# Optimization experiments

Hardware: AMD Instinct MI355X
Metric: run time of the kernel (lower is better)

The kernel has to match this reference:

```python
import jax, jax.numpy as jnp
import numpy as np

B, S, H = 4, 2048, 1024
HEADS = 16
DFF = 4 * H
EPS = 1e-12


def _layer_norm(x, w, b):
    mu = jnp.mean(x, axis=-1, keepdims=True)
    var = jnp.mean(jnp.square(x - mu), axis=-1, keepdims=True)
    return (x - mu) * jax.lax.rsqrt(var + EPS) * w + b


def setup_inputs() -> dict:
    key = jax.random.key(0)
    ks = jax.random.split(key, 12)
    sc = 0.02
    return {
        "input": jax.random.normal(ks[0], (B, S, H), dtype=jnp.float32),
        "input_mask": jnp.zeros((B, 1, 1, S), dtype=jnp.float32),
        "norm_w": jnp.ones((H,), jnp.float32),
        "norm_b": jnp.zeros((H,), jnp.float32),
        "qkv_w": sc * jax.random.normal(ks[1], (H, 3 * H), jnp.float32),
        "qkv_b": jnp.zeros((3 * H,), jnp.float32),
        "attn_ow": sc * jax.random.normal(ks[2], (H, H), jnp.float32),
        "attn_ob": jnp.zeros((H,), jnp.float32),
        "attn_nw": jnp.ones((H,), jnp.float32),
        "attn_nb": jnp.zeros((H,), jnp.float32),
        "inter_w": sc * jax.random.normal(ks[3], (H, DFF), jnp.float32),
        "inter_b": jnp.zeros((DFF,), jnp.float32),
        "output_w": sc * jax.random.normal(ks[4], (DFF, H), jnp.float32),
        "output_b": jnp.zeros((H,), jnp.float32),
    }


def reference(input, input_mask, norm_w, norm_b, qkv_w, qkv_b, attn_ow, attn_ob,
              attn_nw, attn_nb, inter_w, inter_b, output_w, output_b):
    b, s, h = input.shape
    hd = h // HEADS
    # pre-LN + fused QKV projection (qkv_func)
    x_ln = _layer_norm(input, norm_w, norm_b)
    qkv = x_ln @ qkv_w + qkv_b                      # [b, s, 3h]
    qkv = qkv.reshape(b, s, 3, HEADS, hd)
    q, k, v = qkv[:, :, 0], qkv[:, :, 1], qkv[:, :, 2]   # [b, s, heads, hd]
    # scaled dot-product attention (flash_attn equivalent, non-causal)
    scale = 1.0 / jnp.sqrt(jnp.float32(hd))
    scores = jnp.einsum('bqnd,bknd->bnqk', q, k) * scale  # [b, heads, s, s]
    scores = scores + input_mask                           # additive mask
    probs = jax.nn.softmax(scores, axis=-1)
    ctx = jnp.einsum('bnqk,bknd->bqnd', probs, v).reshape(b, s, h)
    # attention output projection + residual (mlp_func first half)
    attn_out = ctx @ attn_ow + attn_ob + input
    # post-attention LN + FFN (GELU) + residual
    y = _layer_norm(attn_out, attn_nw, attn_nb)
    y = jax.nn.gelu(y @ inter_w + inter_b, approximate=False)
    return y @ output_w + output_b + attn_out
```

## Files before the change

### kernel.cpp

```cpp
#include <hip/hip_runtime.h>
#include <math.h>

typedef __bf16 bf16_t;
typedef bf16_t bf16x8 __attribute__((ext_vector_type(8)));
typedef bf16_t bf16x4 __attribute__((ext_vector_type(4)));
typedef float f32x4 __attribute__((ext_vector_type(4)));
typedef float f32x16 __attribute__((ext_vector_type(16)));

#define BB 4
#define SS 2048
#define HD1 1024
#define NH 16
#define DFF_ 4096

__device__ __forceinline__ void gload_lds16(const bf16_t* g, bf16_t* l) {
  __builtin_amdgcn_global_load_lds(
      (const __attribute__((address_space(1))) void*)g,
      (__attribute__((address_space(3))) void*)l, 16, 0, 0);
}

__device__ __forceinline__ unsigned pack2_bf16(float a, float b) {
  union { bf16_t h[2]; unsigned u; } cv;
  cv.h[0] = (bf16_t)a;
  cv.h[1] = (bf16_t)b;
  return cv.u;
}

__device__ __forceinline__ float block_reduce_sum(float v, float* red) {
  const int lane = threadIdx.x & 63;
  const int wid = threadIdx.x >> 6;
#pragma unroll
  for (int off = 32; off > 0; off >>= 1) v += __shfl_down(v, off, 64);
  if (lane == 0) red[wid] = v;
  __syncthreads();
  float s = red[0] + red[1] + red[2] + red[3];
  __syncthreads();
  return s;
}

__global__ __launch_bounds__(256) void ln_kernel(const float* __restrict__ x,
                                                 const float* __restrict__ w,
                                                 const float* __restrict__ bv,
                                                 bf16_t* __restrict__ out) {
  __shared__ float red[4];
  const size_t row = blockIdx.x;
  const float4 xv = *(const float4*)(x + row * HD1 + threadIdx.x * 4);
  float s = xv.x + xv.y + xv.z + xv.w;
  s = block_reduce_sum(s, red);
  const float mu = s * (1.0f / HD1);
  float4 d;
  d.x = xv.x - mu; d.y = xv.y - mu; d.z = xv.z - mu; d.w = xv.w - mu;
  float sq = d.x * d.x + d.y * d.y + d.z * d.z + d.w * d.w;
  sq = block_reduce_sum(sq, red);
  const float rs = rsqrtf(sq * (1.0f / HD1) + 1e-12f);
  const float4 wv = *(const float4*)(w + threadIdx.x * 4);
  const float4 bb = *(const float4*)(bv + threadIdx.x * 4);
  bf16x4 o;
  o[0] = (bf16_t)(d.x * rs * wv.x + bb.x);
  o[1] = (bf16_t)(d.y * rs * wv.y + bb.y);
  o[2] = (bf16_t)(d.z * rs * wv.z + bb.z);
  o[3] = (bf16_t)(d.w * rs * wv.w + bb.w);
  *(bf16x4*)(out + row * HD1 + threadIdx.x * 4) = o;
}

__global__ __launch_bounds__(256) void wt_kernel(const float* __restrict__ W,
                                                 bf16_t* __restrict__ Wt,
                                                 int K, int N) {
  __shared__ bf16_t T[32][33];
  const int t = threadIdx.x;
  const int n0 = blockIdx.x * 32, k0 = blockIdx.y * 32;
  const int a = t >> 5, c = t & 31;
#pragma unroll
  for (int i = 0; i < 4; ++i) {
    const int kl = a + i * 8;
    T[kl][c] = (bf16_t)W[(size_t)(k0 + kl) * N + n0 + c];
  }
  __syncthreads();
#pragma unroll
  for (int i = 0; i < 4; ++i) {
    const int nl = a + i * 8;
    Wt[(size_t)(n0 + nl) * K + k0 + c] = T[c][nl];
  }
}

__global__ __launch_bounds__(256) void vtrans_kernel(const bf16_t* __restrict__ qkv,
                                                     bf16_t* __restrict__ Vt) {
  const int t = threadIdx.x;
  const int s = blockIdx.x * 256 + t;
  const int head = blockIdx.y, b = blockIdx.z;
  const bf16_t* src = qkv + (size_t)(b * SS + s) * 3072 + 2048 + head * 64;
  bf16_t* dst = Vt + ((size_t)(b * NH + head) * 64) * SS + s;
#pragma unroll
  for (int j = 0; j < 8; ++j) {
    bf16x8 v = *(const bf16x8*)(src + j * 8);
#pragma unroll
    for (int e = 0; e < 8; ++e) dst[(size_t)(j * 8 + e) * SS] = v[e];
  }
}

template <int EPI, bool OBF>
__global__ __launch_bounds__(256) void gemm_bf16(
    const bf16_t* __restrict__ A, const bf16_t* __restrict__ Wt,
    const float* __restrict__ bias, const float* __restrict__ R,
    void* __restrict__ Cout, int M, int N, int K) {
  __shared__ __align__(16) char smem[65536];
  bf16_t* As = (bf16_t*)smem;
  bf16_t* Bs = (bf16_t*)(smem + 32768);
  const int tid = threadIdx.x;
  const int lane = tid & 63;
  const int w = tid >> 6;
  const int wm = (w >> 1) * 64, wn = (w & 1) * 64;
  const int l15 = lane & 15, l4 = lane >> 4;

  const int gx = gridDim.x;
  int id = blockIdx.x + gx * blockIdx.y;
  const int cpx = (gx * gridDim.y) >> 3;
  id = (id & 7) * cpx + (id >> 3);
  const int m0 = (id / gx) * 128;
  const int n0 = (id % gx) * 128;

  const int lrow = tid >> 3;
  const int lcol = (tid & 7) * 8;
  const bf16_t* Ag = A + (size_t)(m0 + lrow) * K + lcol;
  const bf16_t* Bg = Wt + (size_t)(n0 + lrow) * K + lcol;
  const size_t rstride = (size_t)32 * K;

#pragma unroll
  for (int c = 0; c < 4; ++c) {
    gload_lds16(Ag + c * rstride, As + c * 2048 + w * 512);
    gload_lds16(Bg + c * rstride, Bs + c * 2048 + w * 512);
  }

  const int NT = K >> 6;
  f32x4 acc[4][4] = {};

  for (int t = 0; t < NT; ++t) {
    const int cur = t & 1;
    __syncthreads();
    if (t + 1 < NT) {
      const bf16_t* Agn = Ag + (size_t)(t + 1) * 64;
      const bf16_t* Bgn = Bg + (size_t)(t + 1) * 64;
      bf16_t* Ad = As + (cur ^ 1) * 8192;
      bf16_t* Bd = Bs + (cur ^ 1) * 8192;
#pragma unroll
      for (int c = 0; c < 4; ++c) {
        gload_lds16(Agn + c * rstride, Ad + c * 2048 + w * 512);
        gload_lds16(Bgn + c * rstride, Bd + c * 2048 + w * 512);
      }
    }
    const bf16_t* Ab = As + cur * 8192;
    const bf16_t* Bb = Bs + cur * 8192;
    bf16x8 af[2][4], bfr[2][4];
#pragma unroll
    for (int ks = 0; ks < 2; ++ks) {
#pragma unroll
      for (int i = 0; i < 4; ++i)
        af[ks][i] =
            *(const bf16x8*)(Ab + (wm + i * 16 + l15) * 64 + ks * 32 + l4 * 8);
#pragma unroll
      for (int j = 0; j < 4; ++j)
        bfr[ks][j] =
            *(const bf16x8*)(Bb + (wn + j * 16 + l15) * 64 + ks * 32 + l4 * 8);
    }
#pragma unroll
    for (int ks = 0; ks < 2; ++ks)
#pragma unroll
      for (int i = 0; i < 4; ++i)
#pragma unroll
        for (int j = 0; j < 4; ++j)
          acc[i][j] = __builtin_amdgcn_mfma_f32_16x16x32_bf16(
              af[ks][i], bfr[ks][j], acc[i][j], 0, 0, 0);
  }

  if (OBF) {
    __syncthreads();
    float* Cs = (float*)smem;
#pragma unroll
    for (int j = 0; j < 4; ++j) {
      const float bj = bias[n0 + wn + j * 16 + l15];
#pragma unroll
      for (int i = 0; i < 4; ++i)
#pragma unroll
        for (int r = 0; r < 4; ++r) {
          float v = acc[i][j][r] + bj;
          if (EPI == 1)
            v = 0.5f * v * (1.0f + erff(v * 0.70710678118654752440f));
          Cs[(wm + i * 16 + l4 * 4 + r) * 128 + wn + j * 16 + l15] = v;
        }
    }
    __syncthreads();
    bf16_t* Cb = (bf16_t*)Cout;
#pragma unroll
    for (int p = 0; p < 16; ++p) {
      const int idx = p * 256 + tid;
      const int row = idx >> 5, c4 = idx & 31;
      const f32x4 v = *(const f32x4*)(Cs + row * 128 + c4 * 4);
      bf16x4 o;
      o[0] = (bf16_t)v[0]; o[1] = (bf16_t)v[1];
      o[2] = (bf16_t)v[2]; o[3] = (bf16_t)v[3];
      *(bf16x4*)(Cb + (size_t)(m0 + row) * N + n0 + c4 * 4) = o;
    }
  } else {
    float* Cf = (float*)Cout;
#pragma unroll
    for (int j = 0; j < 4; ++j) {
      const int gn = n0 + wn + j * 16 + l15;
      const float bj = bias[gn];
#pragma unroll
      for (int i = 0; i < 4; ++i) {
        const int gm = m0 + wm + i * 16 + l4 * 4;
#pragma unroll
        for (int r = 0; r < 4; ++r) {
          float v = acc[i][j][r] + bj;
          if (EPI == 2) v += R[(size_t)(gm + r) * N + gn];
          Cf[(size_t)(gm + r) * N + gn] = v;
        }
      }
    }
  }
}

__global__ __launch_bounds__(256, 2) void attn_kernel(
    const bf16_t* __restrict__ qkv, const bf16_t* __restrict__ Vt,
    const float* __restrict__ mask, bf16_t* __restrict__ ctx) {
  __shared__ __align__(16) bf16_t K_lds[64 * 72];
  __shared__ __align__(16) bf16_t Vt_lds[64 * 72];
  const int tid = threadIdx.x;
  const int lane = tid & 63;
  const int w = tid >> 6;
  const int l31 = lane & 31;
  const int h = lane >> 5;
  const int q0 = blockIdx.x * 128;
  const int head = blockIdx.y;
  const int b = blockIdx.z;
  const int qrow = q0 + w * 32 + l31;

  bf16x8 qf[4];
  {
    const bf16_t* qp = qkv + (size_t)(b * SS + qrow) * 3072 + head * 64 + 8 * h;
#pragma unroll
    for (int ks = 0; ks < 4; ++ks) qf[ks] = *(const bf16x8*)(qp + 16 * ks);
  }

  const int srow = tid >> 2;
  const int scol = (tid & 3) * 16;

  float m = -3.0e38f, l = 0.0f;
  f32x16 cacc0 = {};
  f32x16 cacc1 = {};

  for (int kv0 = 0; kv0 < SS; kv0 += 64) {
    const bf16_t* kp =
        qkv + (size_t)(b * SS + kv0 + srow) * 3072 + 1024 + head * 64 + scol;
    const bf16_t* vp =
        Vt + ((size_t)(b * NH + head) * 64 + srow) * SS + kv0 + scol;
    const bf16x8 k0 = *(const bf16x8*)kp;
    const bf16x8 k1 = *(const bf16x8*)(kp + 8);
    const bf16x8 v0 = *(const bf16x8*)vp;
    const bf16x8 v1 = *(const bf16x8*)(vp + 8);
    float4 mv[8];
#pragma unroll
    for (int k2 = 0; k2 < 8; ++k2)
      mv[k2] = *(const float4*)(mask + (size_t)b * SS + kv0 + 8 * k2 + 4 * h);
    __syncthreads();
    *(bf16x8*)(K_lds + srow * 72 + scol) = k0;
    *(bf16x8*)(K_lds + srow * 72 + scol + 8) = k1;
    *(bf16x8*)(Vt_lds + srow * 72 + scol) = v0;
    *(bf16x8*)(Vt_lds + srow * 72 + scol + 8) = v1;
    __syncthreads();

    f32x16 sacc0 = {};
    f32x16 sacc1 = {};
#pragma unroll
    for (int ks = 0; ks < 4; ++ks) {
      const bf16x8 kf0 = *(const bf16x8*)(K_lds + l31 * 72 + 16 * ks + 8 * h);
      const bf16x8 kf1 =
          *(const bf16x8*)(K_lds + (l31 + 32) * 72 + 16 * ks + 8 * h);
      sacc0 = __builtin_amdgcn_mfma_f32_32x32x16_bf16(kf0, qf[ks], sacc0, 0, 0, 0);
      sacc1 = __builtin_amdgcn_mfma_f32_32x32x16_bf16(kf1, qf[ks], sacc1, 0, 0, 0);
    }

    float ps[32];
    float tmax = -3.0e38f;
#pragma unroll
    for (int r = 0; r < 16; ++r) {
      const float s0 = sacc0[r] * 0.125f + mv[(r >> 2)][r & 3];
      const float s1 = sacc1[r] * 0.125f + mv[(r >> 2) + 4][r & 3];
      ps[r] = s0;
      ps[16 + r] = s1;
      tmax = fmaxf(tmax, fmaxf(s0, s1));
    }
    tmax = fmaxf(tmax, __shfl_xor(tmax, 32, 64));
    if (__any(tmax > m + 8.0f)) {
      const float mnew = fmaxf(m, tmax);
      const float sc = __expf(m - mnew);
      m = mnew;
      l *= sc;
#pragma unroll
      for (int r = 0; r < 16; ++r) {
        const float scr = __shfl(sc, (r & 3) + 8 * (r >> 2) + 4 * h, 64);
        cacc0[r] *= scr;
        cacc1[r] *= scr;
      }
    }
    float ls = 0.0f;
#pragma unroll
    for (int i = 0; i < 32; ++i) {
      ps[i] = __expf(ps[i] - m);
      ls += ps[i];
    }
    l += ls + __shfl_xor(ls, 32, 64);

    unsigned pw0[8], pw1[8];
#pragma unroll
    for (int k = 0; k < 8; ++k) {
      const int base = (k >> 2) * 16 + (k & 3) * 4;
      pw0[k] = pack2_bf16(ps[base + 0], ps[base + 1]);
      pw1[k] = pack2_bf16(ps[base + 2], ps[base + 3]);
    }
#pragma unroll
    for (int t = 0; t < 4; ++t) {
      const unsigned e0 = h ? pw0[2 * t] : pw0[2 * t + 1];
      const unsigned e1 = h ? pw1[2 * t] : pw1[2 * t + 1];
      const unsigned o0 = (unsigned)__shfl_xor((int)e0, 32, 64);
      const unsigned o1 = (unsigned)__shfl_xor((int)e1, 32, 64);
      const unsigned a0 = h ? pw0[2 * t + 1] : pw0[2 * t];
      const unsigned a1 = h ? pw1[2 * t + 1] : pw1[2 * t];
      union { unsigned u[4]; bf16x8 v; } pu;
      pu.u[0] = h ? o0 : a0;
      pu.u[1] = h ? o1 : a1;
      pu.u[2] = h ? a0 : o0;
      pu.u[3] = h ? a1 : o1;
      const bf16x8 vf0 = *(const bf16x8*)(Vt_lds + l31 * 72 + 16 * t + 8 * h);
      const bf16x8 vf1 =
          *(const bf16x8*)(Vt_lds + (l31 + 32) * 72 + 16 * t + 8 * h);
      cacc0 = __builtin_amdgcn_mfma_f32_32x32x16_bf16(pu.v, vf0, cacc0, 0, 0, 0);
      cacc1 = __builtin_amdgcn_mfma_f32_32x32x16_bf16(pu.v, vf1, cacc1, 0, 0, 0);
    }
  }

  const float linv = 1.0f / l;
#pragma unroll
  for (int r = 0; r < 16; ++r) {
    const int rq = (r & 3) + 8 * (r >> 2) + 4 * h;
    const float li = __shfl(linv, rq, 64);
    const int grow = q0 + w * 32 + rq;
    bf16_t* op = ctx + (size_t)(b * SS + grow) * 1024 + head * 64 + l31;
    op[0] = (bf16_t)(cacc0[r] * li);
    op[32] = (bf16_t)(cacc1[r] * li);
  }
}

extern "C" void kernel_launch(void* const* d_in, const int* in_sizes, int n_in,
                              void* d_out, int out_size, void* d_ws, size_t ws_size,
                              hipStream_t stream) {
  const float* input    = (const float*)d_in[0];
  const float* mask     = (const float*)d_in[1];
  const float* norm_w   = (const float*)d_in[2];
  const float* norm_b   = (const float*)d_in[3];
  const float* qkv_w    = (const float*)d_in[4];
  const float* qkv_b    = (const float*)d_in[5];
  const float* attn_ow  = (const float*)d_in[6];
  const float* attn_ob  = (const float*)d_in[7];
  const float* attn_nw  = (const float*)d_in[8];
  const float* attn_nb  = (const float*)d_in[9];
  const float* inter_w  = (const float*)d_in[10];
  const float* inter_b  = (const float*)d_in[11];
  const float* output_w = (const float*)d_in[12];
  const float* output_b = (const float*)d_in[13];

  char* ws = (char*)d_ws;
  const size_t off_xln = 0;
  const size_t off_qkv = 16777216;
  const size_t off_vt  = 67108864;
  const size_t off_ctx = 83886080;
  const size_t off_ao  = 100663296;
  const size_t off_wq  = 134217728;
  const size_t off_wo  = 140509184;
  const size_t off_wi  = 142606336;
  const size_t off_w2  = 150994944;
  const size_t NEED    = 159383552;
  if (ws_size < NEED) return;

  bf16_t* x_ln  = (bf16_t*)(ws + off_xln);
  bf16_t* qkvb  = (bf16_t*)(ws + off_qkv);
  bf16_t* VtB   = (bf16_t*)(ws + off_vt);
  bf16_t* ctxb  = (bf16_t*)(ws + off_ctx);
  bf16_t* y_ln  = (bf16_t*)(ws + off_ctx);
  float*  a_out = (float*)(ws + off_ao);
  bf16_t* wq_t  = (bf16_t*)(ws + off_wq);
  bf16_t* wo_t  = (bf16_t*)(ws + off_wo);
  bf16_t* wi_t  = (bf16_t*)(ws + off_wi);
  bf16_t* w2_t  = (bf16_t*)(ws + off_w2);
  bf16_t* act   = (bf16_t*)(ws + off_xln);

  const int M = BB * SS;

  wt_kernel<<<dim3(3072 / 32, 1024 / 32), 256, 0, stream>>>(qkv_w, wq_t, 1024, 3072);
  wt_kernel<<<dim3(1024 / 32, 1024 / 32), 256, 0, stream>>>(attn_ow, wo_t, 1024, 1024);
  wt_kernel<<<dim3(4096 / 32, 1024 / 32), 256, 0, stream>>>(inter_w, wi_t, 1024, 4096);
  wt_kernel<<<dim3(1024 / 32, 4096 / 32), 256, 0, stream>>>(output_w, w2_t, 4096, 1024);

  ln_kernel<<<M, 256, 0, stream>>>(input, norm_w, norm_b, x_ln);
  gemm_bf16<0, true><<<dim3(3072 / 128, M / 128), 256, 0, stream>>>(
      x_ln, wq_t, qkv_b, nullptr, qkvb, M, 3072, 1024);
  vtrans_kernel<<<dim3(SS / 256, NH, BB), 256, 0, stream>>>(qkvb, VtB);
  attn_kernel<<<dim3(SS / 128, NH, BB), 256, 0, stream>>>(qkvb, VtB, mask, ctxb);
  gemm_bf16<2, false><<<dim3(1024 / 128, M / 128), 256, 0, stream>>>(
      ctxb, wo_t, attn_ob, input, a_out, M, 1024, 1024);
  ln_kernel<<<M, 256, 0, stream>>>(a_out, attn_nw, attn_nb, y_ln);
  gemm_bf16<1, true><<<dim3(4096 / 128, M / 128), 256, 0, stream>>>(
      y_ln, wi_t, inter_b, nullptr, act, M, 4096, 1024);
  gemm_bf16<2, false><<<dim3(1024 / 128, M / 128), 256, 0, stream>>>(
      act, w2_t, output_b, a_out, (float*)d_out, M, 1024, 4096);
}
```

Measured before the change: 499.1 us.

## Templatize GEMM tiles, use 256-row blocks with 512 threads, swizzle epilogue

Makes the bf16 GEMM generic over block tile and warp layout and launches all four projections with 256x128 or 256x256 tiles on 512-thread blocks. Larger tiles raise the arithmetic intensity per LDS load and cut global traffic for the weight and activation operands. The bf16-output epilogue now goes through an XOR-swizzled LDS staging buffer in 128-row passes and writes 16-byte vectors, to reduce bank conflicts and widen the stores. The cost is more LDS (up to 128KB for the 256x256 tile), fewer blocks per CU, and fewer blocks in the grid, which could leave CUs idle.

```diff
diff --git a/kernel.cpp b/kernel.cpp
--- a/kernel.cpp
+++ b/kernel.cpp
@@ -98,117 +98,141 @@
   }
 }
 
-template <int EPI, bool OBF>
-__global__ __launch_bounds__(256) void gemm_bf16(
+template <int BM, int BN, int WM, int WN, int EPI, bool OBF>
+__global__ __launch_bounds__(512) void gemm_bf16(
     const bf16_t* __restrict__ A, const bf16_t* __restrict__ Wt,
     const float* __restrict__ bias, const float* __restrict__ R,
     void* __restrict__ Cout, int M, int N, int K) {
-  __shared__ __align__(16) char smem[65536];
-  bf16_t* As = (bf16_t*)smem;
-  bf16_t* Bs = (bf16_t*)(smem + 32768);
+  constexpr int AST = BM * 64;
+  constexpr int BST = BN * 64;
+  constexpr size_t STAGE_B = (size_t)2 * (AST + BST) * 2;
+  constexpr size_t EPI_B = OBF ? (size_t)128 * BN * 4 : 0;
+  constexpr size_t SMEM_B = STAGE_B > EPI_B ? STAGE_B : EPI_B;
+  __shared__ __align__(16) char smem[SMEM_B];
+  bf16_t* As0 = (bf16_t*)smem;
+  bf16_t* Bs0 = (bf16_t*)smem + 2 * AST;
+
   const int tid = threadIdx.x;
   const int lane = tid & 63;
   const int w = tid >> 6;
-  const int wm = (w >> 1) * 64, wn = (w & 1) * 64;
   const int l15 = lane & 15, l4 = lane >> 4;
+  constexpr int WROWS = BM / WM;
+  constexpr int WCOLS = BN / WN;
+  constexpr int MF = WROWS / 16;
+  constexpr int NF = WCOLS / 16;
+  const int wr = w / WN, wc = w % WN;
+  const int wrow0 = wr * WROWS, wcol0 = wc * WCOLS;
 
   const int gx = gridDim.x;
   int id = blockIdx.x + gx * blockIdx.y;
   const int cpx = (gx * gridDim.y) >> 3;
   id = (id & 7) * cpx + (id >> 3);
-  const int m0 = (id / gx) * 128;
-  const int n0 = (id % gx) * 128;
-
-  const int lrow = tid >> 3;
-  const int lcol = (tid & 7) * 8;
-  const bf16_t* Ag = A + (size_t)(m0 + lrow) * K + lcol;
-  const bf16_t* Bg = Wt + (size_t)(n0 + lrow) * K + lcol;
-  const size_t rstride = (size_t)32 * K;
-
-#pragma unroll
-  for (int c = 0; c < 4; ++c) {
-    gload_lds16(Ag + c * rstride, As + c * 2048 + w * 512);
-    gload_lds16(Bg + c * rstride, Bs + c * 2048 + w * 512);
-  }
+  const int m0 = (id / gx) * BM;
+  const int n0 = (id % gx) * BN;
+
+  const int srow = tid >> 3;
+  const int scol8 = (tid & 7) * 8;
+  const bf16_t* Ag0 = A + (size_t)(m0 + srow) * K + scol8;
+  const bf16_t* Bg0 = Wt + (size_t)(n0 + srow) * K + scol8;
+
+#define STAGE_TILE(T, BUF)                                              \
+  do {                                                                  \
+    const bf16_t* Ag = Ag0 + (size_t)(T)*64;                            \
+    const bf16_t* Bg = Bg0 + (size_t)(T)*64;                            \
+    bf16_t* Ad = As0 + (BUF)*AST + w * 512;                             \
+    bf16_t* Bd = Bs0 + (BUF)*BST + w * 512;                             \
+    _Pragma("unroll") for (int c = 0; c < BM / 64; ++c)                 \
+        gload_lds16(Ag + (size_t)c * 64 * K, Ad + c * 4096);            \
+    _Pragma("unroll") for (int c = 0; c < BN / 64; ++c)                 \
+        gload_lds16(Bg + (size_t)c * 64 * K, Bd + c * 4096);            \
+  } while (0)
+
+  STAGE_TILE(0, 0);
 
   const int NT = K >> 6;
-  f32x4 acc[4][4] = {};
+  f32x4 acc[MF][NF] = {};
 
   for (int t = 0; t < NT; ++t) {
     const int cur = t & 1;
     __syncthreads();
-    if (t + 1 < NT) {
-      const bf16_t* Agn = Ag + (size_t)(t + 1) * 64;
-      const bf16_t* Bgn = Bg + (size_t)(t + 1) * 64;
-      bf16_t* Ad = As + (cur ^ 1) * 8192;
-      bf16_t* Bd = Bs + (cur ^ 1) * 8192;
-#pragma unroll
-      for (int c = 0; c < 4; ++c) {
-        gload_lds16(Agn + c * rstride, Ad + c * 2048 + w * 512);
-        gload_lds16(Bgn + c * rstride, Bd + c * 2048 + w * 512);
+    if (t + 1 < NT) STAGE_TILE(t + 1, cur ^ 1);
+    const bf16_t* Ab = As0 + cur * AST;
+    const bf16_t* Bb = Bs0 + cur * BST;
+#pragma unroll
+    for (int kk = 0; kk < 2; ++kk) {
+      bf16x8 af[MF], bfr[NF];
+#pragma unroll
+      for (int i = 0; i < MF; ++i)
+        af[i] = *(const bf16x8*)(Ab + (wrow0 + i * 16 + l15) * 64 + kk * 32 +
+                                 l4 * 8);
+#pragma unroll
+      for (int j = 0; j < NF; ++j)
+        bfr[j] = *(const bf16x8*)(Bb + (wcol0 + j * 16 + l15) * 64 + kk * 32 +
+                                  l4 * 8);
+#pragma unroll
+      for (int i = 0; i < MF; ++i)
+#pragma unroll
+        for (int j = 0; j < NF; ++j)
+          acc[i][j] = __builtin_amdgcn_mfma_f32_16x16x32_bf16(af[i], bfr[j],
+                                                              acc[i][j], 0, 0, 0);
+    }
+  }
+#undef STAGE_TILE
+
+  if (OBF) {
+    float* Cs = (float*)smem;
+    bf16_t* Cb = (bf16_t*)Cout;
+    constexpr int NP = BM / 128;
+#pragma unroll
+    for (int p = 0; p < NP; ++p) {
+      __syncthreads();
+#pragma unroll
+      for (int i = 0; i < MF; ++i) {
+        const int fr0 = wrow0 + i * 16;
+        if ((fr0 >> 7) == p) {
+#pragma unroll
+          for (int j = 0; j < NF; ++j) {
+            const int col = wcol0 + j * 16 + l15;
+            const float bj = bias[n0 + col];
+#pragma unroll
+            for (int r = 0; r < 4; ++r) {
+              float v = acc[i][j][r] + bj;
+              if (EPI == 1)
+                v = 0.5f * v * (1.0f + erff(v * 0.70710678118654752440f));
+              const int lr = (fr0 & 127) + l4 * 4 + r;
+              const int q = ((col >> 2) ^ (lr & 7)) << 2;
+              Cs[lr * BN + q + (col & 3)] = v;
+            }
+          }
+        }
       }
-    }
-    const bf16_t* Ab = As + cur * 8192;
-    const bf16_t* Bb = Bs + cur * 8192;
-    bf16x8 af[2][4], bfr[2][4];
-#pragma unroll
-    for (int ks = 0; ks < 2; ++ks) {
-#pragma unroll
-      for (int i = 0; i < 4; ++i)
-        af[ks][i] =
-            *(const bf16x8*)(Ab + (wm + i * 16 + l15) * 64 + ks * 32 + l4 * 8);
-#pragma unroll
-      for (int j = 0; j < 4; ++j)
-        bfr[ks][j] =
-            *(const bf16x8*)(Bb + (wn + j * 16 + l15) * 64 + ks * 32 + l4 * 8);
-    }
-#pragma unroll
-    for (int ks = 0; ks < 2; ++ks)
-#pragma unroll
-      for (int i = 0; i < 4; ++i)
-#pragma unroll
-        for (int j = 0; j < 4; ++j)
-          acc[i][j] = __builtin_amdgcn_mfma_f32_16x16x32_bf16(
-              af[ks][i], bfr[ks][j], acc[i][j], 0, 0, 0);
-  }
-
-  if (OBF) {
-    __syncthreads();
-    float* Cs = (float*)smem;
-#pragma unroll
-    for (int j = 0; j < 4; ++j) {
-      const float bj = bias[n0 + wn + j * 16 + l15];
-#pragma unroll
-      for (int i = 0; i < 4; ++i)
-#pragma unroll
-        for (int r = 0; r < 4; ++r) {
-          float v = acc[i][j][r] + bj;
-          if (EPI == 1)
-            v = 0.5f * v * (1.0f + erff(v * 0.70710678118654752440f));
-          Cs[(wm + i * 16 + l4 * 4 + r) * 128 + wn + j * 16 + l15] = v;
-        }
-    }
-    __syncthreads();
-    bf16_t* Cb = (bf16_t*)Cout;
-#pragma unroll
-    for (int p = 0; p < 16; ++p) {
-      const int idx = p * 256 + tid;
-      const int row = idx >> 5, c4 = idx & 31;
-      const f32x4 v = *(const f32x4*)(Cs + row * 128 + c4 * 4);
-      bf16x4 o;
-      o[0] = (bf16_t)v[0]; o[1] = (bf16_t)v[1];
-      o[2] = (bf16_t)v[2]; o[3] = (bf16_t)v[3];
-      *(bf16x4*)(Cb + (size_t)(m0 + row) * N + n0 + c4 * 4) = o;
+      __syncthreads();
+      const int orow = tid >> 2;
+      const int oc = tid & 3;
+#pragma unroll
+      for (int k = 0; k < BN / 32; ++k) {
+        const int col = k * 32 + oc * 8;
+        const int q0 = ((col >> 2) ^ (orow & 7)) << 2;
+        const int q1 = (((col + 4) >> 2) ^ (orow & 7)) << 2;
+        const f32x4 v0 = *(const f32x4*)(Cs + orow * BN + q0);
+        const f32x4 v1 = *(const f32x4*)(Cs + orow * BN + q1);
+        bf16x8 o;
+        o[0] = (bf16_t)v0[0]; o[1] = (bf16_t)v0[1];
+        o[2] = (bf16_t)v0[2]; o[3] = (bf16_t)v0[3];
+        o[4] = (bf16_t)v1[0]; o[5] = (bf16_t)v1[1];
+        o[6] = (bf16_t)v1[2]; o[7] = (bf16_t)v1[3];
+        *(bf16x8*)(Cb + (size_t)(m0 + p * 128 + orow) * N + n0 + col) = o;
+      }
     }
   } else {
     float* Cf = (float*)Cout;
 #pragma unroll
-    for (int j = 0; j < 4; ++j) {
-      const int gn = n0 + wn + j * 16 + l15;
+    for (int j = 0; j < NF; ++j) {
+      const int gn = n0 + wcol0 + j * 16 + l15;
       const float bj = bias[gn];
 #pragma unroll
-      for (int i = 0; i < 4; ++i) {
-        const int gm = m0 + wm + i * 16 + l4 * 4;
+      for (int i = 0; i < MF; ++i) {
+        const int gm = m0 + wrow0 + i * 16 + l4 * 4;
 #pragma unroll
         for (int r = 0; r < 4; ++r) {
           float v = acc[i][j][r] + bj;
@@ -402,15 +426,15 @@
   wt_kernel<<<dim3(1024 / 32, 4096 / 32), 256, 0, stream>>>(output_w, w2_t, 4096, 1024);
 
   ln_kernel<<<M, 256, 0, stream>>>(input, norm_w, norm_b, x_ln);
-  gemm_bf16<0, true><<<dim3(3072 / 128, M / 128), 256, 0, stream>>>(
+  gemm_bf16<256, 128, 4, 2, 0, true><<<dim3(3072 / 128, M / 256), 512, 0, stream>>>(
       x_ln, wq_t, qkv_b, nullptr, qkvb, M, 3072, 1024);
   vtrans_kernel<<<dim3(SS / 256, NH, BB), 256, 0, stream>>>(qkvb, VtB);
   attn_kernel<<<dim3(SS / 128, NH, BB), 256, 0, stream>>>(qkvb, VtB, mask, ctxb);
-  gemm_bf16<2, false><<<dim3(1024 / 128, M / 128), 256, 0, stream>>>(
+  gemm_bf16<256, 128, 4, 2, 2, false><<<dim3(1024 / 128, M / 256), 512, 0, stream>>>(
       ctxb, wo_t, attn_ob, input, a_out, M, 1024, 1024);
   ln_kernel<<<M, 256, 0, stream>>>(a_out, attn_nw, attn_nb, y_ln);
-  gemm_bf16<1, true><<<dim3(4096 / 128, M / 128), 256, 0, stream>>>(
+  gemm_bf16<256, 256, 2, 4, 1, true><<<dim3(4096 / 256, M / 256), 512, 0, stream>>>(
       y_ln, wi_t, inter_b, nullptr, act, M, 4096, 1024);
-  gemm_bf16<2, false><<<dim3(1024 / 128, M / 128), 256, 0, stream>>>(
+  gemm_bf16<256, 128, 4, 2, 2, false><<<dim3(1024 / 128, M / 256), 512, 0, stream>>>(
       act, w2_t, output_b, a_out, (float*)d_out, M, 1024, 4096);
 }
```

Measured after the change: 734.8 us. 47.2% more time.

## Replace GEMM with 8-wave 128x256 ping-pong pipelined kernel with swizzled LDS

Applied to the files above, without the earlier changes.

Replaces the 4-wave 128x128 double-buffered GEMM with a 512-thread kernel computing 128x256 tiles. The K loop is split into fine-grained phases that interleave global-to-LDS loads, LDS fragment reads and MFMA blocks, using explicit barriers, vmcnt/lgkmcnt waits and s_setprio. LDS layouts are XOR-swizzled to avoid bank conflicts, and the bf16 epilogue is staged in two halves with swizzled LDS and 16-byte stores. This aims to hide memory latency and raise MFMA utilisation, at the cost of 96KB of LDS (lower occupancy) and fragile hand-tuned wait counts.

```diff
diff --git a/kernel.cpp b/kernel.cpp
--- a/kernel.cpp
+++ b/kernel.cpp
@@ -98,117 +98,183 @@
   }
 }
 
+#define BAR() __builtin_amdgcn_s_barrier()
+#define LGKM0()                                         \
+  do {                                                  \
+    asm volatile("s_waitcnt lgkmcnt(0)" ::: "memory");  \
+    __builtin_amdgcn_sched_barrier(0);                  \
+  } while (0)
+#define VM4 asm volatile("s_waitcnt vmcnt(4)" ::: "memory")
+#define VM0 asm volatile("s_waitcnt vmcnt(0)" ::: "memory")
+#define PRIO1 __builtin_amdgcn_s_setprio(1)
+#define PRIO0 __builtin_amdgcn_s_setprio(0)
+
 template <int EPI, bool OBF>
-__global__ __launch_bounds__(256) void gemm_bf16(
+__global__ __launch_bounds__(512) void gemm8p(
     const bf16_t* __restrict__ A, const bf16_t* __restrict__ Wt,
     const float* __restrict__ bias, const float* __restrict__ R,
     void* __restrict__ Cout, int M, int N, int K) {
-  __shared__ __align__(16) char smem[65536];
+  __shared__ __align__(16) char smem[98304];
   bf16_t* As = (bf16_t*)smem;
   bf16_t* Bs = (bf16_t*)(smem + 32768);
+
   const int tid = threadIdx.x;
   const int lane = tid & 63;
   const int w = tid >> 6;
-  const int wm = (w >> 1) * 64, wn = (w & 1) * 64;
   const int l15 = lane & 15, l4 = lane >> 4;
+  const int wr = w >> 2;
+  const int wc = w & 3;
+  const int bh = wc >> 1;
+  const int bro = (wc & 1) * 64;
 
   const int gx = gridDim.x;
   int id = blockIdx.x + gx * blockIdx.y;
   const int cpx = (gx * gridDim.y) >> 3;
   id = (id & 7) * cpx + (id >> 3);
   const int m0 = (id / gx) * 128;
-  const int n0 = (id % gx) * 128;
-
-  const int lrow = tid >> 3;
-  const int lcol = (tid & 7) * 8;
-  const bf16_t* Ag = A + (size_t)(m0 + lrow) * K + lcol;
-  const bf16_t* Bg = Wt + (size_t)(n0 + lrow) * K + lcol;
-  const size_t rstride = (size_t)32 * K;
-
-#pragma unroll
-  for (int c = 0; c < 4; ++c) {
-    gload_lds16(Ag + c * rstride, As + c * 2048 + w * 512);
-    gload_lds16(Bg + c * rstride, Bs + c * 2048 + w * 512);
-  }
+  const int n0 = (id % gx) * 256;
+
+  const int srow = tid >> 3;
+  const int scol = (((tid & 7) ^ ((tid >> 3) & 7)) * 8);
+  const bf16_t* Ag = A + (size_t)(m0 + srow) * K + scol;
+  const bf16_t* Bg = Wt + (size_t)(n0 + srow) * K + scol;
+  const size_t K64 = (size_t)64 * K;
+
+  const int chA0 = ((l4) ^ (l15 & 7)) * 8;
+  const int chA1 = ((4 + l4) ^ (l15 & 7)) * 8;
+
+#define STA(d, h, t)                                                       \
+  gload_lds16(Ag + (size_t)(h)*64 * K + (size_t)(t)*64,                    \
+              As + (d)*8192 + (h)*4096 + w * 512)
+#define STB(d, h, t)                                                       \
+  do {                                                                     \
+    gload_lds16(Bg + (size_t)(h)*128 * K + (size_t)(t)*64,                 \
+                Bs + (d)*16384 + (h)*8192 + w * 512);                      \
+    gload_lds16(Bg + (size_t)(h)*128 * K + K64 + (size_t)(t)*64,           \
+                Bs + (d)*16384 + (h)*8192 + 4096 + w * 512);               \
+  } while (0)
+
+  bf16x8 af[4][2], bfr[4][2];
+  f32x4 acc[4][4] = {};
+
+#define LDA(cur)                                                           \
+  do {                                                                     \
+    const bf16_t* Ah_ = As + (cur)*8192 + wr * 4096;                       \
+    _Pragma("unroll") for (int i_ = 0; i_ < 4; ++i_) {                     \
+      af[i_][0] = *(const bf16x8*)(Ah_ + (i_ * 16 + l15) * 64 + chA0);     \
+      af[i_][1] = *(const bf16x8*)(Ah_ + (i_ * 16 + l15) * 64 + chA1);     \
+    }                                                                      \
+  } while (0)
+#define LDB(cur, j0)                                                       \
+  do {                                                                     \
+    const bf16_t* Bh_ = Bs + (cur)*16384 + bh * 8192;                      \
+    _Pragma("unroll") for (int j_ = (j0); j_ < (j0) + 2; ++j_) {           \
+      bfr[j_][0] = *(const bf16x8*)(Bh_ + (bro + j_ * 16 + l15) * 64 + chA0); \
+      bfr[j_][1] = *(const bf16x8*)(Bh_ + (bro + j_ * 16 + l15) * 64 + chA1); \
+    }                                                                      \
+  } while (0)
+#define MM(i0, j0)                                                         \
+  do {                                                                     \
+    _Pragma("unroll") for (int ks_ = 0; ks_ < 2; ++ks_)                    \
+    _Pragma("unroll") for (int i_ = 0; i_ < 2; ++i_)                       \
+    _Pragma("unroll") for (int j_ = 0; j_ < 2; ++j_)                       \
+        acc[(i0) + i_][(j0) + j_] = __builtin_amdgcn_mfma_f32_16x16x32_bf16( \
+            af[(i0) + i_][ks_], bfr[(j0) + j_][ks_],                       \
+            acc[(i0) + i_][(j0) + j_], 0, 0, 0);                           \
+  } while (0)
+
+  STA(0, 0, 0); STA(0, 1, 0); STB(0, 0, 0); STB(0, 1, 0);
+  STA(1, 0, 1); STA(1, 1, 1); STB(1, 0, 1);
+  VM4;
+  BAR();
 
   const int NT = K >> 6;
-  f32x4 acc[4][4] = {};
-
-  for (int t = 0; t < NT; ++t) {
-    const int cur = t & 1;
+  const int nIter = NT >> 1;
+  for (int it = 0; it < nIter; ++it) {
+    const int u = 2 * it;
+    const bool lastI = (it == nIter - 1);
+    LDA(0);
+    LDB(0, 0);
+    STB(1, 1, u + 1);
+    BAR(); LGKM0(); PRIO1; MM(0, 0); PRIO0; BAR();
+    LDB(0, 2);
+    if (!lastI) STA(0, 0, u + 2);
+    BAR(); LGKM0(); PRIO1; MM(2, 0); PRIO0; BAR();
+    if (!lastI) STA(0, 1, u + 2);
+    BAR(); PRIO1; MM(0, 2); PRIO0; BAR();
+    if (!lastI) { STB(0, 0, u + 2); VM4; } else { VM0; }
+    BAR(); PRIO1; MM(2, 2); PRIO0; BAR();
+    LDA(1);
+    LDB(1, 0);
+    if (!lastI) STB(0, 1, u + 2);
+    BAR(); LGKM0(); PRIO1; MM(0, 0); PRIO0; BAR();
+    LDB(1, 2);
+    if (!lastI) STA(1, 0, u + 3);
+    BAR(); LGKM0(); PRIO1; MM(2, 0); PRIO0; BAR();
+    if (!lastI) STA(1, 1, u + 3);
+    BAR(); PRIO1; MM(0, 2); PRIO0; BAR();
+    if (!lastI) { STB(1, 0, u + 3); VM4; }
+    BAR(); PRIO1; MM(2, 2); PRIO0; BAR();
+  }
+#undef STA
+#undef STB
+#undef LDA
+#undef LDB
+#undef MM
+
+  if (OBF) {
+    float* Cs = (float*)smem;
+    bf16_t* Cb = (bf16_t*)Cout;
     __syncthreads();
-    if (t + 1 < NT) {
-      const bf16_t* Agn = Ag + (size_t)(t + 1) * 64;
-      const bf16_t* Bgn = Bg + (size_t)(t + 1) * 64;
-      bf16_t* Ad = As + (cur ^ 1) * 8192;
-      bf16_t* Bd = Bs + (cur ^ 1) * 8192;
-#pragma unroll
-      for (int c = 0; c < 4; ++c) {
-        gload_lds16(Agn + c * rstride, Ad + c * 2048 + w * 512);
-        gload_lds16(Bgn + c * rstride, Bd + c * 2048 + w * 512);
+#pragma unroll
+    for (int p = 0; p < 2; ++p) {
+      if (p) __syncthreads();
+      if (wr == p) {
+#pragma unroll
+        for (int i = 0; i < 4; ++i) {
+#pragma unroll
+          for (int j = 0; j < 4; ++j) {
+            const int col = wc * 64 + j * 16 + l15;
+            const float bj = bias[n0 + col];
+#pragma unroll
+            for (int r = 0; r < 4; ++r) {
+              float v = acc[i][j][r] + bj;
+              if (EPI == 1)
+                v = 0.5f * v * (1.0f + erff(v * 0.70710678118654752440f));
+              const int lr = i * 16 + l4 * 4 + r;
+              const int q = (((col >> 2) ^ (lr & 7)) << 2);
+              Cs[lr * 256 + q + (col & 3)] = v;
+            }
+          }
+        }
       }
-    }
-    const bf16_t* Ab = As + cur * 8192;
-    const bf16_t* Bb = Bs + cur * 8192;
-    bf16x8 af[2][4], bfr[2][4];
-#pragma unroll
-    for (int ks = 0; ks < 2; ++ks) {
-#pragma unroll
-      for (int i = 0; i < 4; ++i)
-        af[ks][i] =
-            *(const bf16x8*)(Ab + (wm + i * 16 + l15) * 64 + ks * 32 + l4 * 8);
-#pragma unroll
-      for (int j = 0; j < 4; ++j)
-        bfr[ks][j] =
-            *(const bf16x8*)(Bb + (wn + j * 16 + l15) * 64 + ks * 32 + l4 * 8);
-    }
-#pragma unroll
-    for (int ks = 0; ks < 2; ++ks)
-#pragma unroll
-      for (int i = 0; i < 4; ++i)
-#pragma unroll
-        for (int j = 0; j < 4; ++j)
-          acc[i][j] = __builtin_amdgcn_mfma_f32_16x16x32_bf16(
-              af[ks][i], bfr[ks][j], acc[i][j], 0, 0, 0);
-  }
-
-  if (OBF) {
-    __syncthreads();
-    float* Cs = (float*)smem;
-#pragma unroll
-    for (int j = 0; j < 4; ++j) {
-      const float bj = bias[n0 + wn + j * 16 + l15];
-#pragma unroll
-      for (int i = 0; i < 4; ++i)
-#pragma unroll
-        for (int r = 0; r < 4; ++r) {
-          float v = acc[i][j][r] + bj;
-          if (EPI == 1)
-            v = 0.5f * v * (1.0f + erff(v * 0.70710678118654752440f));
-          Cs[(wm + i * 16 + l4 * 4 + r) * 128 + wn + j * 16 + l15] = v;
-        }
-    }
-    __syncthreads();
-    bf16_t* Cb = (bf16_t*)Cout;
-#pragma unroll
-    for (int p = 0; p < 16; ++p) {
-      const int idx = p * 256 + tid;
-      const int row = idx >> 5, c4 = idx & 31;
-      const f32x4 v = *(const f32x4*)(Cs + row * 128 + c4 * 4);
-      bf16x4 o;
-      o[0] = (bf16_t)v[0]; o[1] = (bf16_t)v[1];
-      o[2] = (bf16_t)v[2]; o[3] = (bf16_t)v[3];
-      *(bf16x4*)(Cb + (size_t)(m0 + row) * N + n0 + c4 * 4) = o;
+      __syncthreads();
+      const int orow = tid >> 3;
+      const int oc = tid & 7;
+#pragma unroll
+      for (int k = 0; k < 4; ++k) {
+        const int col = k * 64 + oc * 8;
+        const int q0 = ((((col >> 2) + 0) ^ (orow & 7)) << 2);
+        const int q1 = ((((col >> 2) + 1) ^ (orow & 7)) << 2);
+        const f32x4 v0 = *(const f32x4*)(Cs + orow * 256 + q0);
+        const f32x4 v1 = *(const f32x4*)(Cs + orow * 256 + q1);
+        bf16x8 o;
+        o[0] = (bf16_t)v0[0]; o[1] = (bf16_t)v0[1];
+        o[2] = (bf16_t)v0[2]; o[3] = (bf16_t)v0[3];
+        o[4] = (bf16_t)v1[0]; o[5] = (bf16_t)v1[1];
+        o[6] = (bf16_t)v1[2]; o[7] = (bf16_t)v1[3];
+        *(bf16x8*)(Cb + (size_t)(m0 + p * 64 + orow) * N + n0 + col) = o;
+      }
     }
   } else {
     float* Cf = (float*)Cout;
 #pragma unroll
     for (int j = 0; j < 4; ++j) {
-      const int gn = n0 + wn + j * 16 + l15;
+      const int gn = n0 + wc * 64 + j * 16 + l15;
       const float bj = bias[gn];
 #pragma unroll
       for (int i = 0; i < 4; ++i) {
-        const int gm = m0 + wm + i * 16 + l4 * 4;
+        const int gm = m0 + wr * 64 + i * 16 + l4 * 4;
 #pragma unroll
         for (int r = 0; r < 4; ++r) {
           float v = acc[i][j][r] + bj;
@@ -402,15 +468,15 @@
   wt_kernel<<<dim3(1024 / 32, 4096 / 32), 256, 0, stream>>>(output_w, w2_t, 4096, 1024);
 
   ln_kernel<<<M, 256, 0, stream>>>(input, norm_w, norm_b, x_ln);
-  gemm_bf16<0, true><<<dim3(3072 / 128, M / 128), 256, 0, stream>>>(
+  gemm8p<0, true><<<dim3(3072 / 256, M / 128), 512, 0, stream>>>(
       x_ln, wq_t, qkv_b, nullptr, qkvb, M, 3072, 1024);
   vtrans_kernel<<<dim3(SS / 256, NH, BB), 256, 0, stream>>>(qkvb, VtB);
   attn_kernel<<<dim3(SS / 128, NH, BB), 256, 0, stream>>>(qkvb, VtB, mask, ctxb);
-  gemm_bf16<2, false><<<dim3(1024 / 128, M / 128), 256, 0, stream>>>(
+  gemm8p<2, false><<<dim3(1024 / 256, M / 128), 512, 0, stream>>>(
       ctxb, wo_t, attn_ob, input, a_out, M, 1024, 1024);
   ln_kernel<<<M, 256, 0, stream>>>(a_out, attn_nw, attn_nb, y_ln);
-  gemm_bf16<1, true><<<dim3(4096 / 128, M / 128), 256, 0, stream>>>(
+  gemm8p<1, true><<<dim3(4096 / 256, M / 128), 512, 0, stream>>>(
       y_ln, wi_t, inter_b, nullptr, act, M, 4096, 1024);
-  gemm_bf16<2, false><<<dim3(1024 / 128, M / 128), 256, 0, stream>>>(
+  gemm8p<2, false><<<dim3(1024 / 256, M / 128), 512, 0, stream>>>(
       act, w2_t, output_b, a_out, (float*)d_out, M, 1024, 4096);
 }
```

After: 547.4 us. +9.7%, slower.

## Halve GEMM K-tile with swizzled LDS layout to raise occupancy

Applied to the files above, without the earlier changes.

The GEMM now stages a K-chunk of 32 instead of 64 per iteration, which halves shared memory to 32 KB. Together with launch bounds of (256, 4), this is meant to let more blocks reside on each CU. The LDS layout gets an XOR swizzle on 16-byte chunks to reduce bank conflicts on fragment reads. The bf16 epilogue is staged in two 64-row halves through a swizzled LDS buffer and written with 16-byte stores. In exchange, there are twice as many barriers per K and less MFMA work between syncs, and the register cap from the launch bounds could cause spills.

```diff
diff --git a/kernel.cpp b/kernel.cpp
--- a/kernel.cpp
+++ b/kernel.cpp
@@ -99,13 +99,13 @@
 }
 
 template <int EPI, bool OBF>
-__global__ __launch_bounds__(256) void gemm_bf16(
+__global__ __launch_bounds__(256, 4) void gemm2p(
     const bf16_t* __restrict__ A, const bf16_t* __restrict__ Wt,
     const float* __restrict__ bias, const float* __restrict__ R,
     void* __restrict__ Cout, int M, int N, int K) {
-  __shared__ __align__(16) char smem[65536];
+  __shared__ __align__(16) char smem[32768];
   bf16_t* As = (bf16_t*)smem;
-  bf16_t* Bs = (bf16_t*)(smem + 32768);
+  bf16_t* Bs = (bf16_t*)(smem + 16384);
   const int tid = threadIdx.x;
   const int lane = tid & 63;
   const int w = tid >> 6;
@@ -119,86 +119,93 @@
   const int m0 = (id / gx) * 128;
   const int n0 = (id % gx) * 128;
 
-  const int lrow = tid >> 3;
-  const int lcol = (tid & 7) * 8;
-  const bf16_t* Ag = A + (size_t)(m0 + lrow) * K + lcol;
-  const bf16_t* Bg = Wt + (size_t)(n0 + lrow) * K + lcol;
-  const size_t rstride = (size_t)32 * K;
-
-#pragma unroll
-  for (int c = 0; c < 4; ++c) {
-    gload_lds16(Ag + c * rstride, As + c * 2048 + w * 512);
-    gload_lds16(Bg + c * rstride, Bs + c * 2048 + w * 512);
-  }
-
-  const int NT = K >> 6;
+  const int srow = tid >> 2;
+  const int scol = ((tid & 3) ^ (srow & 3)) * 8;
+  const bf16_t* Ag = A + (size_t)(m0 + srow) * K + scol;
+  const bf16_t* Bg = Wt + (size_t)(n0 + srow) * K + scol;
+  const size_t K64 = (size_t)64 * K;
+
+#define STAGE(BUF, T)                                                   \
+  do {                                                                  \
+    const bf16_t* Agt = Ag + (size_t)(T)*32;                            \
+    const bf16_t* Bgt = Bg + (size_t)(T)*32;                            \
+    gload_lds16(Agt, As + (BUF)*4096 + w * 512);                        \
+    gload_lds16(Agt + K64, As + (BUF)*4096 + 2048 + w * 512);           \
+    gload_lds16(Bgt, Bs + (BUF)*4096 + w * 512);                        \
+    gload_lds16(Bgt + K64, Bs + (BUF)*4096 + 2048 + w * 512);           \
+  } while (0)
+
+  const int ch = (l4 ^ (l15 & 3)) * 8;
+
   f32x4 acc[4][4] = {};
 
+  STAGE(0, 0);
+
+  const int NT = K >> 5;
   for (int t = 0; t < NT; ++t) {
     const int cur = t & 1;
     __syncthreads();
-    if (t + 1 < NT) {
-      const bf16_t* Agn = Ag + (size_t)(t + 1) * 64;
-      const bf16_t* Bgn = Bg + (size_t)(t + 1) * 64;
-      bf16_t* Ad = As + (cur ^ 1) * 8192;
-      bf16_t* Bd = Bs + (cur ^ 1) * 8192;
-#pragma unroll
-      for (int c = 0; c < 4; ++c) {
-        gload_lds16(Agn + c * rstride, Ad + c * 2048 + w * 512);
-        gload_lds16(Bgn + c * rstride, Bd + c * 2048 + w * 512);
+    if (t + 1 < NT) STAGE(cur ^ 1, t + 1);
+    const bf16_t* Ab = As + cur * 4096;
+    const bf16_t* Bb = Bs + cur * 4096;
+    bf16x8 af[4], bfr[4];
+#pragma unroll
+    for (int i = 0; i < 4; ++i)
+      af[i] = *(const bf16x8*)(Ab + (wm + i * 16 + l15) * 32 + ch);
+#pragma unroll
+    for (int j = 0; j < 4; ++j)
+      bfr[j] = *(const bf16x8*)(Bb + (wn + j * 16 + l15) * 32 + ch);
+#pragma unroll
+    for (int i = 0; i < 4; ++i)
+#pragma unroll
+      for (int j = 0; j < 4; ++j)
+        acc[i][j] = __builtin_amdgcn_mfma_f32_16x16x32_bf16(af[i], bfr[j],
+                                                            acc[i][j], 0, 0, 0);
+  }
+#undef STAGE
+
+  if (OBF) {
+    float* Cs = (float*)smem;
+    bf16_t* Cb = (bf16_t*)Cout;
+#pragma unroll
+    for (int p = 0; p < 2; ++p) {
+      __syncthreads();
+      if ((w >> 1) == p) {
+#pragma unroll
+        for (int i = 0; i < 4; ++i) {
+#pragma unroll
+          for (int j = 0; j < 4; ++j) {
+            const int col = wn + j * 16 + l15;
+            const float bj = bias[n0 + col];
+#pragma unroll
+            for (int r = 0; r < 4; ++r) {
+              float v = acc[i][j][r] + bj;
+              if (EPI == 1)
+                v = 0.5f * v * (1.0f + erff(v * 0.70710678118654752440f));
+              const int lr = i * 16 + l4 * 4 + r;
+              const int q = (((col >> 2) ^ (lr & 7)) << 2);
+              Cs[lr * 128 + q + (col & 3)] = v;
+            }
+          }
+        }
       }
-    }
-    const bf16_t* Ab = As + cur * 8192;
-    const bf16_t* Bb = Bs + cur * 8192;
-    bf16x8 af[2][4], bfr[2][4];
-#pragma unroll
-    for (int ks = 0; ks < 2; ++ks) {
-#pragma unroll
-      for (int i = 0; i < 4; ++i)
-        af[ks][i] =
-            *(const bf16x8*)(Ab + (wm + i * 16 + l15) * 64 + ks * 32 + l4 * 8);
-#pragma unroll
-      for (int j = 0; j < 4; ++j)
-        bfr[ks][j] =
-            *(const bf16x8*)(Bb + (wn + j * 16 + l15) * 64 + ks * 32 + l4 * 8);
-    }
-#pragma unroll
-    for (int ks = 0; ks < 2; ++ks)
-#pragma unroll
-      for (int i = 0; i < 4; ++i)
-#pragma unroll
-        for (int j = 0; j < 4; ++j)
-          acc[i][j] = __builtin_amdgcn_mfma_f32_16x16x32_bf16(
-              af[ks][i], bfr[ks][j], acc[i][j], 0, 0, 0);
-  }
-
-  if (OBF) {
-    __syncthreads();
-    float* Cs = (float*)smem;
-#pragma unroll
-    for (int j = 0; j < 4; ++j) {
-      const float bj = bias[n0 + wn + j * 16 + l15];
-#pragma unroll
-      for (int i = 0; i < 4; ++i)
-#pragma unroll
-        for (int r = 0; r < 4; ++r) {
-          float v = acc[i][j][r] + bj;
-          if (EPI == 1)
-            v = 0.5f * v * (1.0f + erff(v * 0.70710678118654752440f));
-          Cs[(wm + i * 16 + l4 * 4 + r) * 128 + wn + j * 16 + l15] = v;
-        }
-    }
-    __syncthreads();
-    bf16_t* Cb = (bf16_t*)Cout;
-#pragma unroll
-    for (int p = 0; p < 16; ++p) {
-      const int idx = p * 256 + tid;
-      const int row = idx >> 5, c4 = idx & 31;
-      const f32x4 v = *(const f32x4*)(Cs + row * 128 + c4 * 4);
-      bf16x4 o;
-      o[0] = (bf16_t)v[0]; o[1] = (bf16_t)v[1];
-      o[2] = (bf16_t)v[2]; o[3] = (bf16_t)v[3];
-      *(bf16x4*)(Cb + (size_t)(m0 + row) * N + n0 + c4 * 4) = o;
+      __syncthreads();
+      const int orow = tid >> 2;
+      const int oc = tid & 3;
+#pragma unroll
+      for (int k = 0; k < 4; ++k) {
+        const int col = oc * 32 + k * 8;
+        const int q0 = ((((col >> 2) + 0) ^ (orow & 7)) << 2);
+        const int q1 = ((((col >> 2) + 1) ^ (orow & 7)) << 2);
+        const f32x4 v0 = *(const f32x4*)(Cs + orow * 128 + q0);
+        const f32x4 v1 = *(const f32x4*)(Cs + orow * 128 + q1);
+        bf16x8 o;
+        o[0] = (bf16_t)v0[0]; o[1] = (bf16_t)v0[1];
+        o[2] = (bf16_t)v0[2]; o[3] = (bf16_t)v0[3];
+        o[4] = (bf16_t)v1[0]; o[5] = (bf16_t)v1[1];
+        o[6] = (bf16_t)v1[2]; o[7] = (bf16_t)v1[3];
+        *(bf16x8*)(Cb + (size_t)(m0 + p * 64 + orow) * N + n0 + col) = o;
+      }
     }
   } else {
     float* Cf = (float*)Cout;
@@ -402,15 +409,15 @@
   wt_kernel<<<dim3(1024 / 32, 4096 / 32), 256, 0, stream>>>(output_w, w2_t, 4096, 1024);
 
   ln_kernel<<<M, 256, 0, stream>>>(input, norm_w, norm_b, x_ln);
-  gemm_bf16<0, true><<<dim3(3072 / 128, M / 128), 256, 0, stream>>>(
+  gemm2p<0, true><<<dim3(3072 / 128, M / 128), 256, 0, stream>>>(
       x_ln, wq_t, qkv_b, nullptr, qkvb, M, 3072, 1024);
   vtrans_kernel<<<dim3(SS / 256, NH, BB), 256, 0, stream>>>(qkvb, VtB);
   attn_kernel<<<dim3(SS / 128, NH, BB), 256, 0, stream>>>(qkvb, VtB, mask, ctxb);
-  gemm_bf16<2, false><<<dim3(1024 / 128, M / 128), 256, 0, stream>>>(
+  gemm2p<2, false><<<dim3(1024 / 128, M / 128), 256, 0, stream>>>(
       ctxb, wo_t, attn_ob, input, a_out, M, 1024, 1024);
   ln_kernel<<<M, 256, 0, stream>>>(a_out, attn_nw, attn_nb, y_ln);
-  gemm_bf16<1, true><<<dim3(4096 / 128, M / 128), 256, 0, stream>>>(
+  gemm2p<1, true><<<dim3(4096 / 128, M / 128), 256, 0, stream>>>(
       y_ln, wi_t, inter_b, nullptr, act, M, 4096, 1024);
-  gemm_bf16<2, false><<<dim3(1024 / 128, M / 128), 256, 0, stream>>>(
+  gemm2p<2, false><<<dim3(1024 / 128, M / 128), 256, 0, stream>>>(
       act, w2_t, output_b, a_out, (float*)d_out, M, 1024, 4096);
 }
```

Measured after the change: 521.8 us. +4.5%, slower.
